# Kernel tuning notes

Hardware: AMD Instinct MI355X
Metric: run time of the kernel (lower is better)

The kernel has to match this reference:

```python
import jax, jax.numpy as jnp
import numpy as np

TREE_DEPTH = 6
TEMPERATURE = 1.0


def setup_inputs() -> dict:
    key = jax.random.key(0)
    k1, k2, k3, k4, k5 = jax.random.split(key, 5)
    B, D = 8192, 512
    T = 64                      # n_trees
    N = 2 ** TREE_DEPTH - 1    # internal nodes = 63
    L = 2 ** TREE_DEPTH        # leaves = 64
    C = 100                    # classes
    return {
        "x": jax.random.normal(k1, (B, D), dtype=jnp.float32),
        "split_weights": jax.random.normal(k2, (T, N, D), dtype=jnp.float32),
        "split_bias": jax.random.normal(k3, (T, N), dtype=jnp.float32),
        "leaf_logits": jax.random.normal(k4, (T, L, C), dtype=jnp.float32),
        "tree_weights": jax.random.uniform(k5, (T,), dtype=jnp.float32),
    }


def reference(x, split_weights, split_bias, leaf_logits, tree_weights):
    # All node decisions for all trees in one batched GEMM: [B, T, N]
    dec = jax.nn.sigmoid(
        (jnp.einsum("bd,tnd->btn", x, split_weights) + split_bias) / TEMPERATURE
    )
    B = x.shape[0]
    T = split_weights.shape[0]
    L = leaf_logits.shape[1]  # 2 ** TREE_DEPTH
    leaf_ids = jnp.arange(L)
    # Cumulative product of routing probs along each leaf's root-to-leaf path.
    leaf_probs = jnp.ones((B, T, L), dtype=x.dtype)
    for d in range(TREE_DEPTH):
        # ancestor node (level order) of each leaf at this depth
        node_idx = (2 ** d - 1) + (leaf_ids >> (TREE_DEPTH - d))
        # 1 -> right child (prob = dec), 0 -> left child (prob = 1 - dec)
        bit = (leaf_ids >> (TREE_DEPTH - d - 1)) & 1
        dd = dec[:, :, node_idx]  # [B, T, L]
        leaf_probs = leaf_probs * jnp.where(bit.astype(bool), dd, 1.0 - dd)
    tree_out = jax.nn.softmax(leaf_logits, axis=-1)  # [T, L, C]
    # weighted sum over trees of (leaf_probs @ leaf class dists)
    return jnp.einsum("btl,tlc,t->bc", leaf_probs, tree_out, tree_weights)
```

## Files before the change

kernel.cpp:

```cpp
#include <hip/hip_runtime.h>

#define TREES 64
#define NN 63
#define LL 64
#define CC 100
#define CPAD 112
#define DD 512
#define BB 8192

typedef __attribute__((ext_vector_type(8))) _Float16 f16x8;
typedef __attribute__((ext_vector_type(4))) _Float16 f16x4;
typedef __attribute__((ext_vector_type(4))) float floatx4;

#define XH_WS   0
#define SWH_WS  8388608
#define W2T_WS  12582912

__device__ __forceinline__ void gl_lds16(const _Float16* g, char* lds) {
    __builtin_amdgcn_global_load_lds(
        (const __attribute__((address_space(1))) unsigned int*)g,
        (__attribute__((address_space(3))) unsigned int*)lds, 16, 0, 0);
}

__device__ __forceinline__ f16x8 cvt8(const float* s) {
    float4 a = *(const float4*)s, b = *(const float4*)(s + 4);
    f16x8 h;
    h[0]=(_Float16)a.x; h[1]=(_Float16)a.y; h[2]=(_Float16)a.z; h[3]=(_Float16)a.w;
    h[4]=(_Float16)b.x; h[5]=(_Float16)b.y; h[6]=(_Float16)b.z; h[7]=(_Float16)b.w;
    return h;
}

__device__ __forceinline__ float fsig(float x) {
    return __builtin_amdgcn_rcpf(1.f + __expf(-x));
}

__global__ __launch_bounds__(256) void prep_kernel(
    const float* __restrict__ x, const float* __restrict__ sw,
    const float* __restrict__ leaf_logits, const float* __restrict__ tree_w,
    _Float16* __restrict__ xh, _Float16* __restrict__ swh,
    _Float16* __restrict__ w2T, float* __restrict__ out)
{
    if (blockIdx.x < 3072) {
        int i = blockIdx.x * 256 + threadIdx.x;
        if (i < 524288) {
            int tile = i >> 10, cidx = i & 1023;
            int row = cidx >> 3, c = cidx & 7;
            int rb = tile >> 3, kt = tile & 7;
            int gk = kt * 64 + ((c ^ (row & 7)) << 3);
            *(f16x8*)(xh + (size_t)i * 8) = cvt8(x + (size_t)(rb * 128 + row) * DD + gk);
        } else {
            int j = i - 524288;
            if (j < 262144) {
                int tile = j >> 10, cidx = j & 1023;
                int col = cidx >> 3, c = cidx & 7;
                int cb = tile >> 3, kt = tile & 7;
                int tt = col >> 6, node = col & 63;
                f16x8 h = (f16x8)(_Float16)0.f;
                if (node < NN) {
                    int gk = kt * 64 + ((c ^ (col & 7)) << 3);
                    h = cvt8(sw + (size_t)((cb * 2 + tt) * NN + node) * DD + gk);
                }
                *(f16x8*)(swh + (size_t)j * 8) = h;
            }
        }
    } else if (blockIdx.x < 4096) {
        int row  = (blockIdx.x - 3072) * 4 + (threadIdx.x >> 6);
        int lane = threadIdx.x & 63;
        int t = row >> 6, l = row & 63;
        const float* src = leaf_logits + (size_t)row * CC;
        float v0 = (lane < CC)      ? src[lane]      : -1e30f;
        float v1 = (lane + 64 < CC) ? src[lane + 64] : -1e30f;
        float m = fmaxf(v0, v1);
#pragma unroll
        for (int off = 32; off > 0; off >>= 1)
            m = fmaxf(m, __shfl_down(m, off, 64));
        m = __shfl(m, 0, 64);
        float e0 = (lane < CC)      ? __expf(v0 - m) : 0.f;
        float e1 = (lane + 64 < CC) ? __expf(v1 - m) : 0.f;
        float s = e0 + e1;
#pragma unroll
        for (int off = 32; off > 0; off >>= 1)
            s += __shfl_down(s, off, 64);
        s = __shfl(s, 0, 64);
        float scale = tree_w[t] / s;
        _Float16* base = w2T + (size_t)t * CPAD * LL;
#define LSWZ(c) ((((l >> 3) ^ ((c) & 7)) << 3) | (l & 7))
        if (lane < CC)      base[(size_t)lane * LL + LSWZ(lane)]               = (_Float16)(e0 * scale);
        if (lane + 64 < CC) base[(size_t)(lane + 64) * LL + LSWZ(lane + 64)]   = (_Float16)(e1 * scale);
        if (lane < CPAD - CC) base[(size_t)(CC + lane) * LL + LSWZ(CC + lane)] = (_Float16)0.f;
#undef LSWZ
    } else {
        int i = (blockIdx.x - 4096) * 1024 + threadIdx.x * 4;
        *(float4*)(out + i) = make_float4(0.f, 0.f, 0.f, 0.f);
    }
}

#define A_SMEM 24576
__global__ __launch_bounds__(256, 4) void fused_kernel(
    const _Float16* __restrict__ xh,
    const _Float16* __restrict__ swh,
    const float* __restrict__ sb,
    const _Float16* __restrict__ w2T,
    float* __restrict__ out)
{
    __shared__ __align__(16) char smem[A_SMEM];
    _Float16* xs  = (_Float16*)smem;
    _Float16* wl  = (_Float16*)(smem + 8192);
    _Float16* dec = (_Float16*)smem;
    _Float16* lpl = (_Float16*)smem;

    const int tid  = threadIdx.x;
    const int lane = tid & 63;
    const int wid  = tid >> 6;
    const int quad = lane >> 4;
    const int l15  = lane & 15;
    const int rb   = blockIdx.x;
    const int tc   = blockIdx.y;
    const int rb2  = rb >> 1;
    const int half = rb & 1;

    floatx4 oacc2[7];
#pragma unroll
    for (int ni = 0; ni < 7; ++ni) oacc2[ni] = (floatx4)0.f;

    const _Float16* xtile = xh + (size_t)rb2 * 65536 + (size_t)half * 4096;

    for (int tg = 0; tg < 4; ++tg) {
        const int cb = tc * 4 + tg;
        const _Float16* wtile = swh + (size_t)cb * 65536;

        float bias_v[2];
        {
            int mytree = cb * 2 + (wid >> 1);
#pragma unroll
            for (int ni = 0; ni < 2; ++ni) {
                int nd = 32 * (wid & 1) + 16 * ni + l15;
                bias_v[ni] = (nd < NN) ? sb[mytree * NN + nd] : 0.f;
            }
        }

        floatx4 acc[4][2];
#pragma unroll
        for (int i = 0; i < 4; ++i)
#pragma unroll
            for (int j = 0; j < 2; ++j) acc[i][j] = (floatx4)0.f;

        for (int kt = 0; kt < 8; ++kt) {
            __syncthreads();
#pragma unroll
            for (int j = 0; j < 2; ++j)
                gl_lds16(xtile + kt * 8192 + j * 2048 + wid * 512 + lane * 8,
                         smem + j * 4096 + wid * 1024);
#pragma unroll
            for (int j = 0; j < 4; ++j)
                gl_lds16(wtile + kt * 8192 + j * 2048 + wid * 512 + lane * 8,
                         smem + 8192 + j * 4096 + wid * 1024);
            __syncthreads();
#pragma unroll
            for (int ks = 0; ks < 2; ++ks) {
                f16x8 af[4], bf[2];
#pragma unroll
                for (int mi = 0; mi < 4; ++mi) {
                    int r = 16 * mi + l15;
                    af[mi] = *(const f16x8*)&xs[r * 64 + ((((ks << 2) | quad) ^ (r & 7)) << 3)];
                }
#pragma unroll
                for (int ni = 0; ni < 2; ++ni) {
                    int r = 32 * wid + 16 * ni + l15;
                    bf[ni] = *(const f16x8*)&wl[r * 64 + ((((ks << 2) | quad) ^ (r & 7)) << 3)];
                }
#pragma unroll
                for (int mi = 0; mi < 4; ++mi)
#pragma unroll
                    for (int ni = 0; ni < 2; ++ni)
                        acc[mi][ni] = __builtin_amdgcn_mfma_f32_16x16x32_f16(
                            af[mi], bf[ni], acc[mi][ni], 0, 0, 0);
            }
        }
        __syncthreads();

#pragma unroll
        for (int mi = 0; mi < 4; ++mi) {
            int r0 = 16 * mi + 4 * quad;
#pragma unroll
            for (int ni = 0; ni < 2; ++ni) {
                int col = 32 * wid + 16 * ni + l15;
                f16x4 v;
#pragma unroll
                for (int r = 0; r < 4; ++r)
                    v[r] = (_Float16)(acc[mi][ni][r] + bias_v[ni]);
                *(f16x4*)&dec[col * 66 + r0] = v;
            }
        }
        __syncthreads();

        const int u    = tid >> 7;
        const int tt   = (tid >> 6) & 1;
        const int lrow = tid & 63;
        const int tb   = tt * 64;
        f16x8 lpreg[4];
        {
#define SIG(n) fsig((float)dec[(tb + (n)) * 66 + lrow])
            float d0 = SIG(0);
            float p1 = u ? d0 : 1.f - d0;
            float d1 = SIG(1 + u);
#pragma unroll
            for (int b8 = 0; b8 < 4; ++b8) {
                int i4 = b8 >> 1, i3 = b8 & 1;
                float p2 = p1 * (i4 ? d1 : 1.f - d1);
                float d2 = SIG(3 + 2 * u + i4);
                float p3 = p2 * (i3 ? d2 : 1.f - d2);
                float d3 = SIG(7 + 4 * u + b8);
                f16x8 blk;
#pragma unroll
                for (int i2 = 0; i2 < 2; ++i2) {
                    float p4 = p3 * (i2 ? d3 : 1.f - d3);
                    float d4 = SIG(15 + 8 * u + 2 * b8 + i2);
#pragma unroll
                    for (int i1 = 0; i1 < 2; ++i1) {
                        float p5 = p4 * (i1 ? d4 : 1.f - d4);
                        float d5 = SIG(31 + 16 * u + 4 * b8 + 2 * i2 + i1);
                        blk[i2 * 4 + i1 * 2 + 0] = (_Float16)(p5 * (1.f - d5));
                        blk[i2 * 4 + i1 * 2 + 1] = (_Float16)(p5 * d5);
                    }
                }
                lpreg[b8] = blk;
            }
#undef SIG
        }
        __syncthreads();

#pragma unroll
        for (int b8 = 0; b8 < 4; ++b8) {
            int q = u * 4 + b8;
            *(f16x8*)&lpl[tt * 4096 + lrow * 64 + ((q ^ (lrow & 7)) << 3)] = lpreg[b8];
        }
        __syncthreads();

        {
            const int tree0 = cb * 2;
            const int rbase = wid * 16;
#pragma unroll
            for (int t = 0; t < 2; ++t) {
                const _Float16* bp = w2T + (size_t)(tree0 + t) * (CPAD * LL) + (size_t)l15 * 64;
                const _Float16* lplt = lpl + t * 4096;
#pragma unroll
                for (int ks = 0; ks < 2; ++ks) {
                    const int sw = (((ks << 2) | quad) ^ (l15 & 7)) << 3;
                    f16x8 bbv[7], abv;
#pragma unroll
                    for (int ni = 0; ni < 7; ++ni)
                        bbv[ni] = *(const f16x8*)(bp + ni * 16 * 64 + sw);
                    abv = *(const f16x8*)&lplt[(rbase + l15) * 64 + sw];
#pragma unroll
                    for (int ni = 0; ni < 7; ++ni)
                        oacc2[ni] = __builtin_amdgcn_mfma_f32_16x16x32_f16(
                            abv, bbv[ni], oacc2[ni], 0, 0, 0);
                }
            }
        }
    }

    {
        const int rbase2 = rb * 64 + wid * 16 + 4 * quad;
#pragma unroll
        for (int ni = 0; ni < 7; ++ni) {
            int col = 16 * ni + l15;
            if (col < CC) {
#pragma unroll
                for (int r = 0; r < 4; ++r)
                    unsafeAtomicAdd(&out[(size_t)(rbase2 + r) * CC + col],
                                    oacc2[ni][r]);
            }
        }
    }
}

extern "C" void kernel_launch(void* const* d_in, const int* in_sizes, int n_in,
                              void* d_out, int out_size, void* d_ws, size_t ws_size,
                              hipStream_t stream) {
    const float* x  = (const float*)d_in[0];
    const float* sw = (const float*)d_in[1];
    const float* sb = (const float*)d_in[2];
    const float* ll = (const float*)d_in[3];
    const float* tw = (const float*)d_in[4];
    float* out = (float*)d_out;
    _Float16* xh  = (_Float16*)((char*)d_ws + XH_WS);
    _Float16* swh = (_Float16*)((char*)d_ws + SWH_WS);
    _Float16* w2T = (_Float16*)((char*)d_ws + W2T_WS);

    prep_kernel<<<dim3(4896), 256, 0, stream>>>(x, sw, ll, tw, xh, swh, w2T, out);
    fused_kernel<<<dim3(128, 8), 256, 0, stream>>>(xh, swh, sb, w2T, out);
}
```

Before: 170.0 us.

## Process four trees per tile iteration to halve x-tile reloads

Each block now computes decisions for four trees per outer iteration instead of two, loading two split-weight tiles per k-step into a larger shared buffer while the x tile is loaded once. This halves the number of x tile loads and barriers per block and gives each wave a 4x4 MFMA tile for better operand reuse. The cost is more shared memory (40KB) and registers, with occupancy hint lowered from 4 to 3 blocks per CU.

```diff
diff --git a/kernel.cpp b/kernel.cpp
--- a/kernel.cpp
+++ b/kernel.cpp
@@ -95,8 +95,8 @@
     }
 }
 
-#define A_SMEM 24576
-__global__ __launch_bounds__(256, 4) void fused_kernel(
+#define A_SMEM 40960
+__global__ __launch_bounds__(256, 3) void fused_kernel(
     const _Float16* __restrict__ xh,
     const _Float16* __restrict__ swh,
     const float* __restrict__ sb,
@@ -125,25 +125,22 @@
 
     const _Float16* xtile = xh + (size_t)rb2 * 65536 + (size_t)half * 4096;
 
-    for (int tg = 0; tg < 4; ++tg) {
-        const int cb = tc * 4 + tg;
-        const _Float16* wtile = swh + (size_t)cb * 65536;
-
-        float bias_v[2];
-        {
-            int mytree = cb * 2 + (wid >> 1);
-#pragma unroll
-            for (int ni = 0; ni < 2; ++ni) {
-                int nd = 32 * (wid & 1) + 16 * ni + l15;
-                bias_v[ni] = (nd < NN) ? sb[mytree * NN + nd] : 0.f;
-            }
-        }
-
-        floatx4 acc[4][2];
+    for (int tg = 0; tg < 2; ++tg) {
+        const int cb0 = tc * 4 + tg * 2;
+        const int mytree = tc * 8 + tg * 4 + wid;
+
+        float bias_v[4];
+#pragma unroll
+        for (int ni = 0; ni < 4; ++ni) {
+            int nd = 16 * ni + l15;
+            bias_v[ni] = (nd < NN) ? sb[mytree * NN + nd] : 0.f;
+        }
+
+        floatx4 acc[4][4];
 #pragma unroll
         for (int i = 0; i < 4; ++i)
 #pragma unroll
-            for (int j = 0; j < 2; ++j) acc[i][j] = (floatx4)0.f;
+            for (int j = 0; j < 4; ++j) acc[i][j] = (floatx4)0.f;
 
         for (int kt = 0; kt < 8; ++kt) {
             __syncthreads();
@@ -152,27 +149,30 @@
                 gl_lds16(xtile + kt * 8192 + j * 2048 + wid * 512 + lane * 8,
                          smem + j * 4096 + wid * 1024);
 #pragma unroll
-            for (int j = 0; j < 4; ++j)
-                gl_lds16(wtile + kt * 8192 + j * 2048 + wid * 512 + lane * 8,
-                         smem + 8192 + j * 4096 + wid * 1024);
+            for (int cbl = 0; cbl < 2; ++cbl)
+#pragma unroll
+                for (int j = 0; j < 4; ++j)
+                    gl_lds16(swh + (size_t)(cb0 + cbl) * 65536 + kt * 8192
+                                 + j * 2048 + wid * 512 + lane * 8,
+                             smem + 8192 + cbl * 16384 + j * 4096 + wid * 1024);
             __syncthreads();
 #pragma unroll
             for (int ks = 0; ks < 2; ++ks) {
-                f16x8 af[4], bf[2];
+                f16x8 af[4], bf[4];
 #pragma unroll
                 for (int mi = 0; mi < 4; ++mi) {
                     int r = 16 * mi + l15;
                     af[mi] = *(const f16x8*)&xs[r * 64 + ((((ks << 2) | quad) ^ (r & 7)) << 3)];
                 }
 #pragma unroll
-                for (int ni = 0; ni < 2; ++ni) {
-                    int r = 32 * wid + 16 * ni + l15;
+                for (int ni = 0; ni < 4; ++ni) {
+                    int r = 64 * wid + 16 * ni + l15;
                     bf[ni] = *(const f16x8*)&wl[r * 64 + ((((ks << 2) | quad) ^ (r & 7)) << 3)];
                 }
 #pragma unroll
                 for (int mi = 0; mi < 4; ++mi)
 #pragma unroll
-                    for (int ni = 0; ni < 2; ++ni)
+                    for (int ni = 0; ni < 4; ++ni)
                         acc[mi][ni] = __builtin_amdgcn_mfma_f32_16x16x32_f16(
                             af[mi], bf[ni], acc[mi][ni], 0, 0, 0);
             }
@@ -183,8 +183,8 @@
         for (int mi = 0; mi < 4; ++mi) {
             int r0 = 16 * mi + 4 * quad;
 #pragma unroll
-            for (int ni = 0; ni < 2; ++ni) {
-                int col = 32 * wid + 16 * ni + l15;
+            for (int ni = 0; ni < 4; ++ni) {
+                int col = 64 * wid + 16 * ni + l15;
                 f16x4 v;
 #pragma unroll
                 for (int r = 0; r < 4; ++r)
@@ -194,55 +194,54 @@
         }
         __syncthreads();
 
-        const int u    = tid >> 7;
-        const int tt   = (tid >> 6) & 1;
         const int lrow = tid & 63;
-        const int tb   = tt * 64;
-        f16x8 lpreg[4];
+        const int tb   = wid * 64;
+        f16x8 lpreg[8];
         {
 #define SIG(n) fsig((float)dec[(tb + (n)) * 66 + lrow])
             float d0 = SIG(0);
-            float p1 = u ? d0 : 1.f - d0;
-            float d1 = SIG(1 + u);
-#pragma unroll
-            for (int b8 = 0; b8 < 4; ++b8) {
-                int i4 = b8 >> 1, i3 = b8 & 1;
-                float p2 = p1 * (i4 ? d1 : 1.f - d1);
-                float d2 = SIG(3 + 2 * u + i4);
-                float p3 = p2 * (i3 ? d2 : 1.f - d2);
-                float d3 = SIG(7 + 4 * u + b8);
-                f16x8 blk;
-#pragma unroll
-                for (int i2 = 0; i2 < 2; ++i2) {
-                    float p4 = p3 * (i2 ? d3 : 1.f - d3);
-                    float d4 = SIG(15 + 8 * u + 2 * b8 + i2);
-#pragma unroll
-                    for (int i1 = 0; i1 < 2; ++i1) {
-                        float p5 = p4 * (i1 ? d4 : 1.f - d4);
-                        float d5 = SIG(31 + 16 * u + 4 * b8 + 2 * i2 + i1);
-                        blk[i2 * 4 + i1 * 2 + 0] = (_Float16)(p5 * (1.f - d5));
-                        blk[i2 * 4 + i1 * 2 + 1] = (_Float16)(p5 * d5);
+#pragma unroll
+            for (int h = 0; h < 2; ++h) {
+                float p1 = h ? d0 : 1.f - d0;
+                float d1 = SIG(1 + h);
+#pragma unroll
+                for (int b8 = 0; b8 < 4; ++b8) {
+                    int i4 = b8 >> 1, i3 = b8 & 1;
+                    float p2 = p1 * (i4 ? d1 : 1.f - d1);
+                    float d2 = SIG(3 + 2 * h + i4);
+                    float p3 = p2 * (i3 ? d2 : 1.f - d2);
+                    float d3 = SIG(7 + 4 * h + b8);
+                    f16x8 blk;
+#pragma unroll
+                    for (int i2 = 0; i2 < 2; ++i2) {
+                        float p4 = p3 * (i2 ? d3 : 1.f - d3);
+                        float d4 = SIG(15 + 8 * h + 2 * b8 + i2);
+#pragma unroll
+                        for (int i1 = 0; i1 < 2; ++i1) {
+                            float p5 = p4 * (i1 ? d4 : 1.f - d4);
+                            float d5 = SIG(31 + 16 * h + 4 * b8 + 2 * i2 + i1);
+                            blk[i2 * 4 + i1 * 2 + 0] = (_Float16)(p5 * (1.f - d5));
+                            blk[i2 * 4 + i1 * 2 + 1] = (_Float16)(p5 * d5);
+                        }
                     }
-                }
-                lpreg[b8] = blk;
+                    lpreg[h * 4 + b8] = blk;
+                }
             }
 #undef SIG
         }
         __syncthreads();
 
 #pragma unroll
-        for (int b8 = 0; b8 < 4; ++b8) {
-            int q = u * 4 + b8;
-            *(f16x8*)&lpl[tt * 4096 + lrow * 64 + ((q ^ (lrow & 7)) << 3)] = lpreg[b8];
-        }
+        for (int q = 0; q < 8; ++q)
+            *(f16x8*)&lpl[wid * 4096 + lrow * 64 + ((q ^ (lrow & 7)) << 3)] = lpreg[q];
         __syncthreads();
 
         {
-            const int tree0 = cb * 2;
             const int rbase = wid * 16;
 #pragma unroll
-            for (int t = 0; t < 2; ++t) {
-                const _Float16* bp = w2T + (size_t)(tree0 + t) * (CPAD * LL) + (size_t)l15 * 64;
+            for (int t = 0; t < 4; ++t) {
+                const int tree = tc * 8 + tg * 4 + t;
+                const _Float16* bp = w2T + (size_t)tree * (CPAD * LL) + (size_t)l15 * 64;
                 const _Float16* lplt = lpl + t * 4096;
 #pragma unroll
                 for (int ks = 0; ks < 2; ++ks) {
```

Result: slower. 203.2 us (+19.5%).

## Double-buffer LDS tiles to overlap global loads with MFMA compute

Applied to the files above, without the earlier changes.

Doubles shared memory to two 24KB stage buffers. The next K-tile of x and split weights is now issued while the current tile feeds the MFMAs, and the first tile of the next tree group is prefetched during the leaf-logit GEMM phase. This removes one barrier per K-step and hides global-to-LDS load latency. The cost is higher LDS use, so launch bounds drop from 4 to 3 blocks per CU, which lowers occupancy.

```diff
diff --git a/kernel.cpp b/kernel.cpp
--- a/kernel.cpp
+++ b/kernel.cpp
@@ -95,8 +95,9 @@
     }
 }
 
-#define A_SMEM 24576
-__global__ __launch_bounds__(256, 4) void fused_kernel(
+#define SETB 24576
+#define A_SMEM 49152
+__global__ __launch_bounds__(256, 3) void fused_kernel(
     const _Float16* __restrict__ xh,
     const _Float16* __restrict__ swh,
     const float* __restrict__ sb,
@@ -104,10 +105,8 @@
     float* __restrict__ out)
 {
     __shared__ __align__(16) char smem[A_SMEM];
-    _Float16* xs  = (_Float16*)smem;
-    _Float16* wl  = (_Float16*)(smem + 8192);
     _Float16* dec = (_Float16*)smem;
-    _Float16* lpl = (_Float16*)smem;
+    _Float16* lpl = (_Float16*)(smem + SETB);
 
     const int tid  = threadIdx.x;
     const int lane = tid & 63;
@@ -125,6 +124,21 @@
 
     const _Float16* xtile = xh + (size_t)rb2 * 65536 + (size_t)half * 4096;
 
+#define STAGE(WT, KT, SOFF)                                                    \
+    {                                                                          \
+        _Pragma("unroll")                                                      \
+        for (int j = 0; j < 2; ++j)                                            \
+            gl_lds16(xtile + (KT) * 8192 + j * 2048 + wid * 512 + lane * 8,    \
+                     smem + (SOFF) + j * 4096 + wid * 1024);                   \
+        _Pragma("unroll")                                                      \
+        for (int j = 0; j < 4; ++j)                                            \
+            gl_lds16((WT) + (KT) * 8192 + j * 2048 + wid * 512 + lane * 8,     \
+                     smem + (SOFF) + 8192 + j * 4096 + wid * 1024);            \
+    }
+
+    STAGE(swh + (size_t)(tc * 4) * 65536, 0, 0);
+    __syncthreads();
+
     for (int tg = 0; tg < 4; ++tg) {
         const int cb = tc * 4 + tg;
         const _Float16* wtile = swh + (size_t)cb * 65536;
@@ -146,16 +160,11 @@
             for (int j = 0; j < 2; ++j) acc[i][j] = (floatx4)0.f;
 
         for (int kt = 0; kt < 8; ++kt) {
-            __syncthreads();
-#pragma unroll
-            for (int j = 0; j < 2; ++j)
-                gl_lds16(xtile + kt * 8192 + j * 2048 + wid * 512 + lane * 8,
-                         smem + j * 4096 + wid * 1024);
-#pragma unroll
-            for (int j = 0; j < 4; ++j)
-                gl_lds16(wtile + kt * 8192 + j * 2048 + wid * 512 + lane * 8,
-                         smem + 8192 + j * 4096 + wid * 1024);
-            __syncthreads();
+            if (kt < 7)
+                STAGE(wtile, kt + 1, ((kt + 1) & 1) * SETB);
+            const int cur = (kt & 1) * SETB;
+            const _Float16* xs = (const _Float16*)(smem + cur);
+            const _Float16* wl = (const _Float16*)(smem + cur + 8192);
 #pragma unroll
             for (int ks = 0; ks < 2; ++ks) {
                 f16x8 af[4], bf[2];
@@ -176,8 +185,8 @@
                         acc[mi][ni] = __builtin_amdgcn_mfma_f32_16x16x32_f16(
                             af[mi], bf[ni], acc[mi][ni], 0, 0, 0);
             }
-        }
-        __syncthreads();
+            __syncthreads();
+        }
 
 #pragma unroll
         for (int mi = 0; mi < 4; ++mi) {
@@ -228,8 +237,6 @@
             }
 #undef SIG
         }
-        __syncthreads();
-
 #pragma unroll
         for (int b8 = 0; b8 < 4; ++b8) {
             int q = u * 4 + b8;
@@ -237,6 +244,9 @@
         }
         __syncthreads();
 
+        if (tg < 3)
+            STAGE(swh + (size_t)(cb + 1) * 65536, 0, 0);
+
         {
             const int tree0 = cb * 2;
             const int rbase = wid * 16;
@@ -259,7 +269,9 @@
                 }
             }
         }
+        __syncthreads();
     }
+#undef STAGE
 
     {
         const int rbase2 = rb * 64 + wid * 16 + 4 * quad;
```

Result: slower. 179.3 us (+5.5%).

## Triple-buffer GEMM K-loop with async LDS loads and cross-tree-group prefetch

Applied to the files above, without the earlier changes.

Replaces the single-buffered K loop, which did two block barriers per 64-wide K tile, with a 16-step loop over 32-wide K slices. Slices rotate through three LDS buffers, loads are issued two steps ahead, and waits use vmcnt counters before each barrier. The dec and leaf-prob scratch regions move to separate offsets so the first two slices of the next tree group can be prefetched during the leaf-prob and second-GEMM phases. LDS grows from 24KB to 36KB per block, which may reduce occupancy at 4 blocks per CU. Correctness relies on the hand-written vmcnt accounting and the reused LDS regions not overlapping.

```diff
diff --git a/kernel.cpp b/kernel.cpp
--- a/kernel.cpp
+++ b/kernel.cpp
@@ -95,7 +95,10 @@
     }
 }
 
-#define A_SMEM 24576
+#define BUF 12288
+#define A_SMEM 36864
+#define DEC_OFF 0
+#define LPL_OFF 16896
 __global__ __launch_bounds__(256, 4) void fused_kernel(
     const _Float16* __restrict__ xh,
     const _Float16* __restrict__ swh,
@@ -104,10 +107,8 @@
     float* __restrict__ out)
 {
     __shared__ __align__(16) char smem[A_SMEM];
-    _Float16* xs  = (_Float16*)smem;
-    _Float16* wl  = (_Float16*)(smem + 8192);
-    _Float16* dec = (_Float16*)smem;
-    _Float16* lpl = (_Float16*)smem;
+    _Float16* dec = (_Float16*)(smem + DEC_OFF);
+    _Float16* lpl = (_Float16*)(smem + LPL_OFF);
 
     const int tid  = threadIdx.x;
     const int lane = tid & 63;
@@ -125,9 +126,33 @@
 
     const _Float16* xtile = xh + (size_t)rb2 * 65536 + (size_t)half * 4096;
 
+    const int rowp = tid >> 2;
+    const int pp   = tid & 3;
+
+#define STAGE3(WT, KT, KS, SOFF)                                               \
+    {                                                                          \
+        int kcx = (KS) * 4 + (pp ^ ((rowp >> 1) & 3));                         \
+        gl_lds16(xtile + (KT) * 8192 + rowp * 64 + ((kcx ^ (rowp & 7)) << 3),  \
+                 smem + (SOFF) + wid * 1024);                                  \
+        _Pragma("unroll")                                                      \
+        for (int j = 0; j < 2; ++j) {                                          \
+            int colj = j * 64 + rowp;                                          \
+            int kcw = (KS) * 4 + (pp ^ ((colj >> 1) & 3));                     \
+            gl_lds16((WT) + (KT) * 8192 + colj * 64 + ((kcw ^ (colj & 7)) << 3),\
+                     smem + (SOFF) + 4096 + j * 4096 + wid * 1024);            \
+        }                                                                      \
+    }
+
+    {
+        const _Float16* wt0 = swh + (size_t)(tc * 4) * 65536;
+        STAGE3(wt0, 0, 0, 0)
+        STAGE3(wt0, 0, 1, BUF)
+    }
+
     for (int tg = 0; tg < 4; ++tg) {
         const int cb = tc * 4 + tg;
         const _Float16* wtile = swh + (size_t)cb * 65536;
+        const _Float16* wnext = swh + (size_t)(cb + 1) * 65536;
 
         float bias_v[2];
         {
@@ -145,37 +170,35 @@
 #pragma unroll
             for (int j = 0; j < 2; ++j) acc[i][j] = (floatx4)0.f;
 
-        for (int kt = 0; kt < 8; ++kt) {
-            __syncthreads();
-#pragma unroll
-            for (int j = 0; j < 2; ++j)
-                gl_lds16(xtile + kt * 8192 + j * 2048 + wid * 512 + lane * 8,
-                         smem + j * 4096 + wid * 1024);
-#pragma unroll
-            for (int j = 0; j < 4; ++j)
-                gl_lds16(wtile + kt * 8192 + j * 2048 + wid * 512 + lane * 8,
-                         smem + 8192 + j * 4096 + wid * 1024);
-            __syncthreads();
-#pragma unroll
-            for (int ks = 0; ks < 2; ++ks) {
-                f16x8 af[4], bf[2];
-#pragma unroll
-                for (int mi = 0; mi < 4; ++mi) {
-                    int r = 16 * mi + l15;
-                    af[mi] = *(const f16x8*)&xs[r * 64 + ((((ks << 2) | quad) ^ (r & 7)) << 3)];
-                }
-#pragma unroll
-                for (int ni = 0; ni < 2; ++ni) {
-                    int r = 32 * wid + 16 * ni + l15;
-                    bf[ni] = *(const f16x8*)&wl[r * 64 + ((((ks << 2) | quad) ^ (r & 7)) << 3)];
-                }
-#pragma unroll
-                for (int mi = 0; mi < 4; ++mi)
-#pragma unroll
-                    for (int ni = 0; ni < 2; ++ni)
-                        acc[mi][ni] = __builtin_amdgcn_mfma_f32_16x16x32_f16(
-                            af[mi], bf[ni], acc[mi][ni], 0, 0, 0);
-            }
+#pragma unroll
+        for (int s = 0; s < 16; ++s) {
+            if (s == 15) asm volatile("s_waitcnt vmcnt(0)" ::: "memory");
+            else         asm volatile("s_waitcnt vmcnt(3)" ::: "memory");
+            __builtin_amdgcn_s_barrier();
+
+            const int cur = (s % 3) * BUF;
+            const _Float16* xs = (const _Float16*)(smem + cur);
+            const _Float16* wl = (const _Float16*)(smem + cur + 4096);
+            f16x8 af[4], bf[2];
+#pragma unroll
+            for (int mi = 0; mi < 4; ++mi) {
+                int r = 16 * mi + l15;
+                af[mi] = *(const f16x8*)&xs[r * 32 + ((quad ^ ((r >> 1) & 3)) << 3)];
+            }
+#pragma unroll
+            for (int ni = 0; ni < 2; ++ni) {
+                int r = 32 * wid + 16 * ni + l15;
+                bf[ni] = *(const f16x8*)&wl[r * 32 + ((quad ^ ((r >> 1) & 3)) << 3)];
+            }
+#pragma unroll
+            for (int mi = 0; mi < 4; ++mi)
+#pragma unroll
+                for (int ni = 0; ni < 2; ++ni)
+                    acc[mi][ni] = __builtin_amdgcn_mfma_f32_16x16x32_f16(
+                        af[mi], bf[ni], acc[mi][ni], 0, 0, 0);
+
+            if (s <= 13)
+                STAGE3(wtile, (s + 2) >> 1, (s + 2) & 1, ((s + 2) % 3) * BUF)
         }
         __syncthreads();
 
@@ -228,14 +251,15 @@
             }
 #undef SIG
         }
-        __syncthreads();
-
 #pragma unroll
         for (int b8 = 0; b8 < 4; ++b8) {
             int q = u * 4 + b8;
             *(f16x8*)&lpl[tt * 4096 + lrow * 64 + ((q ^ (lrow & 7)) << 3)] = lpreg[b8];
         }
         __syncthreads();
+
+        if (tg < 3)
+            STAGE3(wnext, 0, 0, 0)
 
         {
             const int tree0 = cb * 2;
@@ -259,7 +283,12 @@
                 }
             }
         }
-    }
+        __syncthreads();
+
+        if (tg < 3)
+            STAGE3(wnext, 0, 1, BUF)
+    }
+#undef STAGE3
 
     {
         const int rbase2 = rb * 64 + wid * 16 + 4 * quad;
```

After: 203.4 us. 19.7% more time.
